# Kernel tuning notes

Measured on AMD Instinct MI355X. Metric: run time of the kernel, lower is better.

Reference implementation:

```python
import jax, jax.numpy as jnp
import numpy as np

N_NODES = 40000
N_EDGES = 400000
N_GRAPHS = 64
CONV_DIM = 64
N_FEAT = 9
EDGE_DIM = 3
Z_DIM = 2 * CONV_DIM + EDGE_DIM  # 131


def setup_inputs() -> dict:
    key = jax.random.key(0)
    ks = jax.random.split(key, 32)
    def lin(k, fan_in, fan_out):
        b = 1.0 / np.sqrt(fan_in)
        kw, kb = jax.random.split(k)
        return (jax.random.uniform(kw, (fan_in, fan_out), jnp.float32, -b, b),
                jax.random.uniform(kb, (fan_out,), jnp.float32, -b, b))
    inp = {}
    inp['x'] = jax.random.normal(ks[0], (N_NODES, N_FEAT), jnp.float32)
    inp['edge_index_1'] = jax.random.randint(ks[1], (2, N_EDGES), 0, N_NODES, jnp.int32)
    inp['edge_index_2'] = jax.random.randint(ks[2], (2, N_EDGES), 0, N_NODES, jnp.int32)
    inp['weight_1'] = jax.random.normal(ks[3], (N_EDGES, EDGE_DIM), jnp.float32)
    inp['weight_2'] = jax.random.normal(ks[4], (N_EDGES, EDGE_DIM), jnp.float32)
    # sorted graph ids: 64 graphs of 625 nodes each
    inp['batch'] = jnp.repeat(jnp.arange(N_GRAPHS, dtype=jnp.int32), N_NODES // N_GRAPHS)
    # parameters (stored [in, out])
    inp['fc1_w'], inp['fc1_b'] = lin(ks[5], N_FEAT, CONV_DIM)
    inp['lin_f_w'], inp['lin_f_b'] = lin(ks[6], Z_DIM, CONV_DIM)
    inp['lin_s_w'], inp['lin_s_b'] = lin(ks[7], Z_DIM, CONV_DIM)
    inp['gru_w_ih'], inp['gru_b_ih'] = lin(ks[8], CONV_DIM, 3 * CONV_DIM)  # gate order r,z,n
    inp['gru_w_hh'], inp['gru_b_hh'] = lin(ks[9], CONV_DIM, 3 * CONV_DIM)
    inp['fcs_w'], inp['fcs_b'] = lin(ks[10], CONV_DIM, CONV_DIM)
    inp['fc2c_w'], inp['fc2c_b'] = lin(ks[11], CONV_DIM, 64)
    inp['fc3c_w'], inp['fc3c_b'] = lin(ks[12], 64, 2)
    inp['fc2d_w'], inp['fc2d_b'] = lin(ks[13], CONV_DIM, 64)
    inp['fc3d_w'], inp['fc3d_b'] = lin(ks[14], 64, 2)
    return inp


def _cgconv(x, edge_index, edge_attr, wf, bf, ws, bs):
    # CGConv, flow='target_to_source': x_i = x[row], x_j = x[col], aggregate (mean) at row
    row, col = edge_index[0], edge_index[1]
    z = jnp.concatenate([x[row], x[col], edge_attr], axis=-1)       # [E, 131]
    msg = jax.nn.sigmoid(z @ wf + bf) * jax.nn.softplus(z @ ws + bs)  # [E, C]
    agg = jax.ops.segment_sum(msg, row, num_segments=x.shape[0])
    cnt = jax.ops.segment_sum(jnp.ones((msg.shape[0],), msg.dtype), row, num_segments=x.shape[0])
    return x + agg / jnp.maximum(cnt, 1.0)[:, None]                  # residual


def _gru_step(xt, h, w_ih, w_hh, b_ih, b_hh):
    gi = xt @ w_ih + b_ih
    gh = h @ w_hh + b_hh
    ir, iz, inn = jnp.split(gi, 3, axis=-1)
    hr, hz, hn = jnp.split(gh, 3, axis=-1)
    r = jax.nn.sigmoid(ir + hr)
    zg = jax.nn.sigmoid(iz + hz)
    n = jnp.tanh(inn + r * hn)
    return (1.0 - zg) * n + zg * h


def reference(x, edge_index_1, edge_index_2, weight_1, weight_2, batch,
              fc1_w, fc1_b, lin_f_w, lin_f_b, lin_s_w, lin_s_b,
              gru_w_ih, gru_b_ih, gru_w_hh, gru_b_hh,
              fcs_w, fcs_b, fc2c_w, fc2c_b, fc3c_w, fc3c_b,
              fc2d_w, fc2d_b, fc3d_w, fc3d_b):
    x = jax.nn.relu(x @ fc1_w + fc1_b)          # dropout inactive (eval)
    h = x
    for _ in range(3):                          # 3 GRU refinement iterations
        m = jax.nn.relu(_cgconv(x, edge_index_2, weight_2, lin_f_w, lin_f_b, lin_s_w, lin_s_b))
        m = jax.nn.relu(_cgconv(m, edge_index_1, weight_1, lin_f_w, lin_f_b, lin_s_w, lin_s_b))
        h = _gru_step(m, h, gru_w_ih, gru_w_hh, gru_b_ih, gru_b_hh)
        x = h
    # first node index of each graph (batch is sorted)
    idx_ct = jnp.searchsorted(batch, jnp.arange(N_GRAPHS, dtype=batch.dtype))
    xg = x[idx_ct]                              # [B, C]
    xg = jax.nn.relu(xg @ fcs_w + fcs_b)
    xc = jax.nn.relu(xg @ fc2c_w + fc2c_b)
    x_class = jax.nn.sigmoid(xc @ fc3c_w + fc3c_b)
    xd = jax.nn.relu(xg @ fc2d_w + fc2d_b)
    x_delta = xd @ fc3d_w + fc3d_b
    return (x_class, x_delta)
```

## Files before the change

kernel.cpp:

```cpp
#include <hip/hip_runtime.h>
#include <hip/hip_bf16.h>
#include <hip/hip_fp16.h>
#include <math.h>

constexpr int NE = 400000;
constexpr int NN = 40000;
constexpr int CD = 64;
constexpr int NGRAPH = 64;
constexpr int SCAN_BLOCKS = (NN + 255) / 256;
constexpr int EBLK = (NE + 255) / 256;

typedef _Float16 f16x8 __attribute__((ext_vector_type(8)));
typedef float f32x4 __attribute__((ext_vector_type(4)));

__global__ void k_fc1(const float* __restrict__ x,
                      const float* __restrict__ w,
                      const float* __restrict__ b,
                      float* __restrict__ out) {
    int i = blockIdx.x * 256 + threadIdx.x;
    if (i >= NN * CD) return;
    int n = i >> 6, c = i & 63;
    float acc = b[c];
    #pragma unroll
    for (int k = 0; k < 9; ++k)
        acc = fmaf(x[n * 9 + k], w[k * 64 + c], acc);
    out[i] = fmaxf(acc, 0.f);
}

__global__ void k_count2(const int* __restrict__ ei1, const int* __restrict__ ei2,
                         int* __restrict__ cnt1, int* __restrict__ cnt2) {
    const int b = blockIdx.x;
    const bool s2 = (b >= EBLK);
    const int* ei = s2 ? ei2 : ei1;
    int* cnt = s2 ? cnt2 : cnt1;
    int e = (s2 ? b - EBLK : b) * 256 + threadIdx.x;
    if (e >= NE) return;
    atomicAdd(&cnt[ei[e]], 1);
}

__global__ void k_scan_part2(const int* __restrict__ cnt1, const int* __restrict__ cnt2,
                             int* __restrict__ part1, int* __restrict__ part2) {
    __shared__ int red[256];
    const int b = blockIdx.x;
    const bool s2 = (b >= SCAN_BLOCKS);
    const int* cnt = s2 ? cnt2 : cnt1;
    int* partials = s2 ? part2 : part1;
    const int bb = s2 ? b - SCAN_BLOCKS : b;
    const int tid = threadIdx.x;
    const int i = bb * 256 + tid;
    red[tid] = (i < NN) ? cnt[i] : 0;
    __syncthreads();
    for (int s = 128; s > 0; s >>= 1) {
        if (tid < s) red[tid] += red[tid + s];
        __syncthreads();
    }
    if (tid == 0) partials[bb] = red[0];
}

__global__ void k_scan_mid2(const int* __restrict__ part1, const int* __restrict__ part2,
                            int* __restrict__ offs1, int* __restrict__ offs2) {
    __shared__ int part[256];
    const bool s2 = (blockIdx.x == 1);
    const int* partials = s2 ? part2 : part1;
    int* offs = s2 ? offs2 : offs1;
    const int tid = threadIdx.x;
    const int v = (tid < SCAN_BLOCKS) ? partials[tid] : 0;
    part[tid] = v;
    __syncthreads();
    for (int off = 1; off < 256; off <<= 1) {
        int t = (tid >= off) ? part[tid - off] : 0;
        __syncthreads();
        part[tid] += t;
        __syncthreads();
    }
    if (tid < SCAN_BLOCKS) offs[tid] = part[tid] - v;
}

__global__ void k_scan_fill2(const int* __restrict__ cnt1, const int* __restrict__ cnt2,
                             const int* __restrict__ offs1, const int* __restrict__ offs2,
                             int* __restrict__ rs1, int* __restrict__ rs2,
                             int* __restrict__ cur1, int* __restrict__ cur2) {
    __shared__ int part[256];
    const int b = blockIdx.x;
    const bool s2 = (b >= SCAN_BLOCKS);
    const int* cnt = s2 ? cnt2 : cnt1;
    const int* offs = s2 ? offs2 : offs1;
    int* row_start = s2 ? rs2 : rs1;
    int* cursor = s2 ? cur2 : cur1;
    const int bb = s2 ? b - SCAN_BLOCKS : b;
    const int tid = threadIdx.x;
    const int i = bb * 256 + tid;
    const int v = (i < NN) ? cnt[i] : 0;
    part[tid] = v;
    __syncthreads();
    for (int off = 1; off < 256; off <<= 1) {
        int t = (tid >= off) ? part[tid - off] : 0;
        __syncthreads();
        part[tid] += t;
        __syncthreads();
    }
    const int excl = part[tid] - v + offs[bb];
    if (i < NN) { row_start[i] = excl; cursor[i] = excl; }
    if (i == NN - 1) row_start[NN] = NE;
}

__global__ void k_scatgath2(const int* __restrict__ ei1, const int* __restrict__ ei2,
                            const float* __restrict__ w1, const float* __restrict__ w2,
                            int* __restrict__ cur1, int* __restrict__ cur2,
                            int2* __restrict__ rcP1, int2* __restrict__ rcP2,
                            float4* __restrict__ ewP1, float4* __restrict__ ewP2) {
    const int b = blockIdx.x;
    const bool s2 = (b >= EBLK);
    const int* ei = s2 ? ei2 : ei1;
    const float* ew = s2 ? w2 : w1;
    int* cursor = s2 ? cur2 : cur1;
    int2* rcP = s2 ? rcP2 : rcP1;
    float4* ewP = s2 ? ewP2 : ewP1;
    int e = (s2 ? b - EBLK : b) * 256 + threadIdx.x;
    if (e >= NE) return;
    const int r = ei[e];
    const int c = ei[NE + e];
    const int pos = atomicAdd(&cursor[r], 1);
    rcP[pos] = make_int2(r, c);
    ewP[pos] = make_float4(ew[3 * e], ew[3 * e + 1], ew[3 * e + 2], 0.f);
}

__global__ void k_wt16(const float* __restrict__ lfw, const float* __restrict__ lsw,
                       _Float16* __restrict__ Wt) {
    const int k = blockIdx.x;
    const int c = threadIdx.x;
    float v;
    if (c < 64)       v = lfw[k * 64 + c];
    else if (c < 128) v = lsw[k * 64 + (c - 64)];
    else if (c < 192) v = lfw[(64 + k) * 64 + (c - 128)];
    else              v = lsw[(64 + k) * 64 + (c - 192)];
    Wt[c * 64 + k] = (_Float16)v;
}

__global__ void k_wtg16(const float* __restrict__ wih, const float* __restrict__ whh,
                        _Float16* __restrict__ WtG) {
    const int i = blockIdx.x * 256 + threadIdx.x;
    const int c = i >> 6, k = i & 63;
    const float v = (c < 192) ? wih[k * 192 + c] : whh[k * 192 + (c - 192)];
    WtG[c * 64 + k] = (_Float16)v;
}

__launch_bounds__(256, 4)
__global__ void k_proj_mfma(const float* __restrict__ x,
                            const _Float16* __restrict__ Wt,
                            const float* __restrict__ bfp, const float* __restrict__ bsp,
                            float* __restrict__ Pi, __half2* __restrict__ Pj16) {
    __shared__ _Float16 xs16[32][72];
    const int tid = threadIdx.x;
    const int n0 = blockIdx.x * 32;
    {
        const int n = tid >> 3, k0 = (tid & 7) * 8;
        const float4 a = *(const float4*)&x[(size_t)(n0 + n) * 64 + k0];
        const float4 b = *(const float4*)&x[(size_t)(n0 + n) * 64 + k0 + 4];
        f16x8 v;
        v[0] = (_Float16)a.x; v[1] = (_Float16)a.y; v[2] = (_Float16)a.z; v[3] = (_Float16)a.w;
        v[4] = (_Float16)b.x; v[5] = (_Float16)b.y; v[6] = (_Float16)b.z; v[7] = (_Float16)b.w;
        *(f16x8*)&xs16[n][k0] = v;
    }
    __syncthreads();
    const int l  = tid & 63;
    const int w  = tid >> 6;
    const int lr = l & 15;
    const int kb = l >> 4;
    const int nt = w & 1;
    const f16x8 A0 = *(const f16x8*)&xs16[nt * 16 + lr][kb * 8];
    const f16x8 A1 = *(const f16x8*)&xs16[nt * 16 + lr][32 + kb * 8];
    const int orow = n0 + nt * 16 + kb * 4;

    if (w < 2) {
        for (int ct = 0; ct < 8; ++ct) {
            const int col = ct * 16 + lr;
            const f16x8 B0 = *(const f16x8*)&Wt[col * 64 + kb * 8];
            const f16x8 B1 = *(const f16x8*)&Wt[col * 64 + 32 + kb * 8];
            f32x4 acc = {0.f, 0.f, 0.f, 0.f};
            acc = __builtin_amdgcn_mfma_f32_16x16x32_f16(A0, B0, acc, 0, 0, 0);
            acc = __builtin_amdgcn_mfma_f32_16x16x32_f16(A1, B1, acc, 0, 0, 0);
            const float bias = (col < 64) ? bfp[col] : bsp[col - 64];
            #pragma unroll
            for (int r = 0; r < 4; ++r)
                Pi[(size_t)(orow + r) * 128 + col] = acc[r] + bias;
        }
    } else {
        for (int pt = 0; pt < 4; ++pt) {
            const int colF = 128 + pt * 16 + lr;
            const int colS = 192 + pt * 16 + lr;
            const f16x8 BF0 = *(const f16x8*)&Wt[colF * 64 + kb * 8];
            const f16x8 BF1 = *(const f16x8*)&Wt[colF * 64 + 32 + kb * 8];
            const f16x8 BS0 = *(const f16x8*)&Wt[colS * 64 + kb * 8];
            const f16x8 BS1 = *(const f16x8*)&Wt[colS * 64 + 32 + kb * 8];
            f32x4 aF = {0.f, 0.f, 0.f, 0.f}, aS = {0.f, 0.f, 0.f, 0.f};
            aF = __builtin_amdgcn_mfma_f32_16x16x32_f16(A0, BF0, aF, 0, 0, 0);
            aF = __builtin_amdgcn_mfma_f32_16x16x32_f16(A1, BF1, aF, 0, 0, 0);
            aS = __builtin_amdgcn_mfma_f32_16x16x32_f16(A0, BS0, aS, 0, 0, 0);
            aS = __builtin_amdgcn_mfma_f32_16x16x32_f16(A1, BS1, aS, 0, 0, 0);
            const int cj = pt * 16 + lr;
            #pragma unroll
            for (int r = 0; r < 4; ++r)
                Pj16[(size_t)(orow + r) * 64 + cj] = __floats2half2_rn((float)aF[r], (float)aS[r]);
        }
    }
}

__launch_bounds__(256, 8)
__global__ void k_edge_range(const __half2* __restrict__ Pj,
                             const float* __restrict__ Pi,
                             const int2* __restrict__ rcP, const float4* __restrict__ ewP,
                             const float* __restrict__ wfe, const float* __restrict__ wse,
                             const int* __restrict__ rs,
                             const float* __restrict__ xin, float* __restrict__ out) {
    __shared__ __align__(8) __half2 piH[8][64];
    __shared__ __align__(16) float accS[8][8][64];
    __shared__ int rsS[9];
    const int tid = threadIdx.x;
    const int hw = tid >> 5;
    const int hb = hw & 1;
    const int wv = tid >> 6;
    const int c2 = (tid & 31) * 2;
    const int r0 = blockIdx.x * 8;
    for (int i = tid; i < 512; i += 256) {
        const int row = i >> 6, ch = i & 63;
        piH[row][ch] = __floats2half2_rn(Pi[(size_t)(r0 + row) * 128 + ch],
                                         Pi[(size_t)(r0 + row) * 128 + 64 + ch]);
    }
    for (int i = tid; i < 4096; i += 256)
        ((float*)accS)[i] = 0.f;
    if (tid < 9) rsS[tid] = rs[r0 + tid];
    __syncthreads();
    const float wf0a = wfe[c2],       wf0b = wfe[c2 + 1];
    const float wf1a = wfe[64 + c2],  wf1b = wfe[64 + c2 + 1];
    const float wf2a = wfe[128 + c2], wf2b = wfe[128 + c2 + 1];
    const float ws0a = wse[c2],       ws0b = wse[c2 + 1];
    const float ws1a = wse[64 + c2],  ws1b = wse[64 + c2 + 1];
    const float ws2a = wse[128 + c2], ws2b = wse[128 + c2 + 1];
    const int pbeg = rsS[0], pend = rsS[8];

#define EDGE_BODY(P)                                                              \
    {                                                                             \
        const int2 rc = rcP[P];                                                   \
        const float4 e = ewP[P];                                                  \
        const uint2 Jraw = *(const uint2*)&Pj[rc.y * 64 + c2];                    \
        const float2 Ja = __half22float2(*(const __half2*)&Jraw.x);               \
        const float2 Jb = __half22float2(*(const __half2*)&Jraw.y);               \
        const int row = rc.x - r0;                                                \
        const uint2 PH = *(const uint2*)&piH[row][c2];                            \
        const float2 Pa = __half22float2(*(const __half2*)&PH.x);                 \
        const float2 Pb = __half22float2(*(const __half2*)&PH.y);                 \
        const float afa = Pa.x + Ja.x + e.x * wf0a + e.y * wf1a + e.z * wf2a;     \
        const float asa = Pa.y + Ja.y + e.x * ws0a + e.y * ws1a + e.z * ws2a;     \
        const float afb = Pb.x + Jb.x + e.x * wf0b + e.y * wf1b + e.z * wf2b;     \
        const float asb = Pb.y + Jb.y + e.x * ws0b + e.y * ws1b + e.z * ws2b;     \
        const float sga = 1.f / (1.f + __expf(-afa));                             \
        const float spa = (asa > 20.f) ? asa : __logf(1.f + __expf(asa));         \
        const float sgb = 1.f / (1.f + __expf(-afb));                             \
        const float spb = (asb > 20.f) ? asb : __logf(1.f + __expf(asb));         \
        float2 acc = *(const float2*)&accS[hw][row][c2];                          \
        acc.x = fmaf(sga, spa, acc.x);                                            \
        acc.y = fmaf(sgb, spb, acc.y);                                            \
        *(float2*)&accS[hw][row][c2] = acc;                                       \
    }

    int p0 = pbeg + 2 * wv;
    #pragma unroll 2
    for (; p0 + 2 <= pend; p0 += 8) {
        const int p = p0 + hb;
        EDGE_BODY(p)
    }
    {
        const int p = p0 + hb;
        if (p < pend) EDGE_BODY(p)
    }
#undef EDGE_BODY

    __syncthreads();
    for (int i = tid; i < 512; i += 256) {
        const int row = i >> 6, ch = i & 63;
        float s = 0.f;
        #pragma unroll
        for (int a = 0; a < 8; ++a) s += accS[a][row][ch];
        const int deg = rsS[row + 1] - rsS[row];
        const size_t o = (size_t)(r0 + row) * 64 + ch;
        out[o] = fmaxf(fmaf(s, 1.f / (float)max(deg, 1), xin[o]), 0.f);
    }
}

__global__ void k_gru_mfma(const float* __restrict__ m, float* __restrict__ h,
                           const _Float16* __restrict__ WtG,
                           const float* __restrict__ bih, const float* __restrict__ bhh) {
    __shared__ _Float16 ms16[32][72];
    __shared__ _Float16 hs16[32][72];
    __shared__ __align__(16) float hs32[32][64];
    const int tid = threadIdx.x;
    const int n0 = blockIdx.x * 32;
    {
        const int n = tid >> 3, k0 = (tid & 7) * 8;
        const float4 ma = *(const float4*)&m[(size_t)(n0 + n) * 64 + k0];
        const float4 mb = *(const float4*)&m[(size_t)(n0 + n) * 64 + k0 + 4];
        const float4 ha = *(const float4*)&h[(size_t)(n0 + n) * 64 + k0];
        const float4 hb = *(const float4*)&h[(size_t)(n0 + n) * 64 + k0 + 4];
        f16x8 mv, hv;
        mv[0] = (_Float16)ma.x; mv[1] = (_Float16)ma.y; mv[2] = (_Float16)ma.z; mv[3] = (_Float16)ma.w;
        mv[4] = (_Float16)mb.x; mv[5] = (_Float16)mb.y; mv[6] = (_Float16)mb.z; mv[7] = (_Float16)mb.w;
        hv[0] = (_Float16)ha.x; hv[1] = (_Float16)ha.y; hv[2] = (_Float16)ha.z; hv[3] = (_Float16)ha.w;
        hv[4] = (_Float16)hb.x; hv[5] = (_Float16)hb.y; hv[6] = (_Float16)hb.z; hv[7] = (_Float16)hb.w;
        *(f16x8*)&ms16[n][k0] = mv;
        *(f16x8*)&hs16[n][k0] = hv;
        *(float4*)&hs32[n][k0] = ha;
        *(float4*)&hs32[n][k0 + 4] = hb;
    }
    __syncthreads();
    const int l  = tid & 63;
    const int w  = tid >> 6;
    const int lr = l & 15;
    const int kb = l >> 4;
    const int nt = w & 1;
    const int cg = w >> 1;
    const f16x8 A0 = *(const f16x8*)&ms16[nt * 16 + lr][kb * 8];
    const f16x8 A1 = *(const f16x8*)&ms16[nt * 16 + lr][32 + kb * 8];
    const f16x8 H0 = *(const f16x8*)&hs16[nt * 16 + lr][kb * 8];
    const f16x8 H1 = *(const f16x8*)&hs16[nt * 16 + lr][32 + kb * 8];
    const int orow = n0 + nt * 16 + kb * 4;
    const int lrow = nt * 16 + kb * 4;

    #pragma unroll
    for (int t = 0; t < 2; ++t) {
        const int ct = cg + t * 2;
        const int c = ct * 16 + lr;
        const f16x8 BiR0 = *(const f16x8*)&WtG[(c)       * 64 + kb * 8];
        const f16x8 BiR1 = *(const f16x8*)&WtG[(c)       * 64 + 32 + kb * 8];
        const f16x8 BiZ0 = *(const f16x8*)&WtG[(64 + c)  * 64 + kb * 8];
        const f16x8 BiZ1 = *(const f16x8*)&WtG[(64 + c)  * 64 + 32 + kb * 8];
        const f16x8 BiN0 = *(const f16x8*)&WtG[(128 + c) * 64 + kb * 8];
        const f16x8 BiN1 = *(const f16x8*)&WtG[(128 + c) * 64 + 32 + kb * 8];
        const f16x8 BhR0 = *(const f16x8*)&WtG[(192 + c) * 64 + kb * 8];
        const f16x8 BhR1 = *(const f16x8*)&WtG[(192 + c) * 64 + 32 + kb * 8];
        const f16x8 BhZ0 = *(const f16x8*)&WtG[(256 + c) * 64 + kb * 8];
        const f16x8 BhZ1 = *(const f16x8*)&WtG[(256 + c) * 64 + 32 + kb * 8];
        const f16x8 BhN0 = *(const f16x8*)&WtG[(320 + c) * 64 + kb * 8];
        const f16x8 BhN1 = *(const f16x8*)&WtG[(320 + c) * 64 + 32 + kb * 8];
        f32x4 aIR = {0,0,0,0}, aIZ = {0,0,0,0}, aIN = {0,0,0,0};
        f32x4 aHR = {0,0,0,0}, aHZ = {0,0,0,0}, aHN = {0,0,0,0};
        aIR = __builtin_amdgcn_mfma_f32_16x16x32_f16(A0, BiR0, aIR, 0, 0, 0);
        aIR = __builtin_amdgcn_mfma_f32_16x16x32_f16(A1, BiR1, aIR, 0, 0, 0);
        aIZ = __builtin_amdgcn_mfma_f32_16x16x32_f16(A0, BiZ0, aIZ, 0, 0, 0);
        aIZ = __builtin_amdgcn_mfma_f32_16x16x32_f16(A1, BiZ1, aIZ, 0, 0, 0);
        aIN = __builtin_amdgcn_mfma_f32_16x16x32_f16(A0, BiN0, aIN, 0, 0, 0);
        aIN = __builtin_amdgcn_mfma_f32_16x16x32_f16(A1, BiN1, aIN, 0, 0, 0);
        aHR = __builtin_amdgcn_mfma_f32_16x16x32_f16(H0, BhR0, aHR, 0, 0, 0);
        aHR = __builtin_amdgcn_mfma_f32_16x16x32_f16(H1, BhR1, aHR, 0, 0, 0);
        aHZ = __builtin_amdgcn_mfma_f32_16x16x32_f16(H0, BhZ0, aHZ, 0, 0, 0);
        aHZ = __builtin_amdgcn_mfma_f32_16x16x32_f16(H1, BhZ1, aHZ, 0, 0, 0);
        aHN = __builtin_amdgcn_mfma_f32_16x16x32_f16(H0, BhN0, aHN, 0, 0, 0);
        aHN = __builtin_amdgcn_mfma_f32_16x16x32_f16(H1, BhN1, aHN, 0, 0, 0);
        const float bir = bih[c], biz = bih[64 + c], bin = bih[128 + c];
        const float bhr = bhh[c], bhz = bhh[64 + c], bhn = bhh[128 + c];
        #pragma unroll
        for (int r = 0; r < 4; ++r) {
            const float rg = 1.f / (1.f + __expf(-(((float)aIR[r] + bir) + ((float)aHR[r] + bhr))));
            const float zg = 1.f / (1.f + __expf(-(((float)aIZ[r] + biz) + ((float)aHZ[r] + bhz))));
            const float ng = tanhf(((float)aIN[r] + bin) + rg * ((float)aHN[r] + bhn));
            h[(size_t)(orow + r) * 64 + c] = (1.f - zg) * ng + zg * hs32[lrow + r][c];
        }
    }
}

__global__ void k_head(const float* __restrict__ h, const int* __restrict__ batch,
                       const float* __restrict__ fcsw, const float* __restrict__ fcsb,
                       const float* __restrict__ f2cw, const float* __restrict__ f2cb,
                       const float* __restrict__ f3cw, const float* __restrict__ f3cb,
                       const float* __restrict__ f2dw, const float* __restrict__ f2db,
                       const float* __restrict__ f3dw, const float* __restrict__ f3db,
                       float* __restrict__ out) {
    __shared__ float hsB[4096];
    __shared__ float waB[4096];
    __shared__ float wbB[4096];
    __shared__ float wcB[4096];
    __shared__ int sidx[64];
    const int tid = threadIdx.x;
    if (tid < 64) {
        int lo = 0, hi = NN;
        while (lo < hi) {
            int mid = (lo + hi) >> 1;
            if (batch[mid] < tid) lo = mid + 1; else hi = mid;
        }
        sidx[tid] = lo;
    }
    __syncthreads();
    for (int i = tid; i < 4096; i += 256) {
        int g = i >> 6, k = i & 63;
        hsB[i] = h[(size_t)sidx[g] * 64 + k];
        waB[i] = fcsw[i];
        wbB[i] = f2cw[i];
        wcB[i] = f2dw[i];
    }
    __syncthreads();
    float v[16];
    #pragma unroll
    for (int j = 0; j < 16; ++j) {
        const int i = j * 256 + tid, g = i >> 6, c = i & 63;
        float a = fcsb[c];
        for (int k = 0; k < 64; ++k) a = fmaf(hsB[g * 64 + k], waB[k * 64 + c], a);
        v[j] = fmaxf(a, 0.f);
    }
    __syncthreads();
    #pragma unroll
    for (int j = 0; j < 16; ++j) hsB[j * 256 + tid] = v[j];
    __syncthreads();
    float vc[16], vd[16];
    #pragma unroll
    for (int j = 0; j < 16; ++j) {
        const int i = j * 256 + tid, g = i >> 6, c = i & 63;
        float a1 = f2cb[c], a2 = f2db[c];
        for (int k = 0; k < 64; ++k) {
            const float xv = hsB[g * 64 + k];
            a1 = fmaf(xv, wbB[k * 64 + c], a1);
            a2 = fmaf(xv, wcB[k * 64 + c], a2);
        }
        vc[j] = fmaxf(a1, 0.f);
        vd[j] = fmaxf(a2, 0.f);
    }
    __syncthreads();
    #pragma unroll
    for (int j = 0; j < 16; ++j) {
        waB[j * 256 + tid] = vc[j];
        wbB[j * 256 + tid] = vd[j];
    }
    if (tid < 128) wcB[tid] = f3cw[tid];
    else           wcB[tid] = f3dw[tid - 128];
    __syncthreads();
    if (tid < 128) {
        int g = tid >> 1, j = tid & 1;
        float a = f3cb[j];
        for (int k = 0; k < 64; ++k) a = fmaf(waB[g * 64 + k], wcB[k * 2 + j], a);
        out[g * 2 + j] = 1.f / (1.f + expf(-a));
    } else {
        int t = tid - 128, g = t >> 1, j = t & 1;
        float a = f3db[j];
        for (int k = 0; k < 64; ++k) a = fmaf(wbB[g * 64 + k], wcB[128 + k * 2 + j], a);
        out[128 + g * 2 + j] = a;
    }
}

extern "C" void kernel_launch(void* const* d_in, const int* in_sizes, int n_in,
                              void* d_out, int out_size, void* d_ws, size_t ws_size,
                              hipStream_t stream) {
    (void)in_sizes; (void)n_in; (void)out_size; (void)ws_size;
    const float* x    = (const float*)d_in[0];
    const int* ei1    = (const int*)d_in[1];
    const int* ei2    = (const int*)d_in[2];
    const float* w1   = (const float*)d_in[3];
    const float* w2   = (const float*)d_in[4];
    const int* batch  = (const int*)d_in[5];
    const float* fc1w = (const float*)d_in[6];
    const float* fc1b = (const float*)d_in[7];
    const float* lfw  = (const float*)d_in[8];
    const float* lfb  = (const float*)d_in[9];
    const float* lsw  = (const float*)d_in[10];
    const float* lsb  = (const float*)d_in[11];
    const float* wih  = (const float*)d_in[12];
    const float* bih  = (const float*)d_in[13];
    const float* whh  = (const float*)d_in[14];
    const float* bhh  = (const float*)d_in[15];
    const float* fcsw = (const float*)d_in[16];
    const float* fcsb = (const float*)d_in[17];
    const float* f2cw = (const float*)d_in[18];
    const float* f2cb = (const float*)d_in[19];
    const float* f3cw = (const float*)d_in[20];
    const float* f3cb = (const float*)d_in[21];
    const float* f2dw = (const float*)d_in[22];
    const float* f2db = (const float*)d_in[23];
    const float* f3dw = (const float*)d_in[24];
    const float* f3db = (const float*)d_in[25];

    char* ws = (char*)d_ws;
    size_t off = 0;
    auto alloc = [&](size_t bytes) { char* p = ws + off; off += (bytes + 255) & ~size_t(255); return p; };
    float*   Pi    = (float*)alloc(size_t(NN) * 128 * 4);
    __half2* Pj16  = (__half2*)alloc(size_t(NN) * 64 * 4);
    float*   hbuf  = (float*)alloc(size_t(NN) * CD * 4);
    float*   mbuf  = (float*)alloc(size_t(NN) * CD * 4);
    _Float16* W16  = (_Float16*)alloc(256 * 64 * 2);
    _Float16* WG16 = (_Float16*)alloc(384 * 64 * 2);
    int*   cnt1  = (int*)alloc(size_t(NN) * 4);
    int*   cnt2  = (int*)alloc(size_t(NN) * 4);
    int*   rs1   = (int*)alloc(size_t(NN + 1) * 4);
    int*   rs2   = (int*)alloc(size_t(NN + 1) * 4);
    int*   cur1  = (int*)alloc(size_t(NN + 1) * 4);
    int*   cur2  = (int*)alloc(size_t(NN + 1) * 4);
    int2*  rcP1  = (int2*)alloc(size_t(NE) * 8);
    int2*  rcP2  = (int2*)alloc(size_t(NE) * 8);
    float4* ewP1 = (float4*)alloc(size_t(NE) * 16);
    float4* ewP2 = (float4*)alloc(size_t(NE) * 16);
    int*   part1 = (int*)alloc(256 * 4);
    int*   part2 = (int*)alloc(256 * 4);
    int*   offs1 = (int*)alloc(256 * 4);
    int*   offs2 = (int*)alloc(256 * 4);

    const int NB_NC = (NN * CD + 255) / 256;
    const int EDGE_BLOCKS = NN / 8;
    const int PROJ_BLOCKS = NN / 32;
    const int GRU_BLOCKS  = NN / 32;

    const float* lfe = lfw + 128 * 64;
    const float* lse = lsw + 128 * 64;

    hipMemsetAsync(cnt1, 0, size_t(NN) * 4 * 2 + 256, stream);
    k_count2<<<2 * EBLK, 256, 0, stream>>>(ei1, ei2, cnt1, cnt2);
    k_scan_part2<<<2 * SCAN_BLOCKS, 256, 0, stream>>>(cnt1, cnt2, part1, part2);
    k_scan_mid2<<<2, 256, 0, stream>>>(part1, part2, offs1, offs2);
    k_scan_fill2<<<2 * SCAN_BLOCKS, 256, 0, stream>>>(cnt1, cnt2, offs1, offs2, rs1, rs2, cur1, cur2);
    k_scatgath2<<<2 * EBLK, 256, 0, stream>>>(ei1, ei2, w1, w2, cur1, cur2,
                                              rcP1, rcP2, ewP1, ewP2);
    k_wt16<<<64, 256, 0, stream>>>(lfw, lsw, W16);
    k_wtg16<<<96, 256, 0, stream>>>(wih, whh, WG16);

    k_fc1<<<NB_NC, 256, 0, stream>>>(x, fc1w, fc1b, hbuf);

    for (int it = 0; it < 3; ++it) {
        k_proj_mfma<<<PROJ_BLOCKS, 256, 0, stream>>>(hbuf, W16, lfb, lsb, Pi, Pj16);
        k_edge_range<<<EDGE_BLOCKS, 256, 0, stream>>>(Pj16, Pi, rcP2, ewP2,
                                                      lfe, lse, rs2, hbuf, mbuf);
        k_proj_mfma<<<PROJ_BLOCKS, 256, 0, stream>>>(mbuf, W16, lfb, lsb, Pi, Pj16);
        k_edge_range<<<EDGE_BLOCKS, 256, 0, stream>>>(Pj16, Pi, rcP1, ewP1,
                                                      lfe, lse, rs1, mbuf, mbuf);
        k_gru_mfma<<<GRU_BLOCKS, 256, 0, stream>>>(mbuf, hbuf, WG16, bih, bhh);
    }

    k_head<<<1, 256, 0, stream>>>(hbuf, batch, fcsw, fcsb, f2cw, f2cb, f3cw, f3cb,
                                  f2dw, f2db, f3dw, f3db, (float*)d_out);
}
```

Before: 563.2 us.

## Pack sorted edge records into compact int and fp16 edge-weight arrays

The CSR preprocessing is split into a scatter pass that writes only an edge permutation and a gather pass that writes packed records sequentially. Each record stores the column index with the row's offset within its 8-row block in the top bits, plus the edge weights as fp16 in 8 bytes instead of a float4. The aim is to cut the per-edge bytes read by the six edge kernels from 24 to 12 and to make the scattered writes smaller. In exchange there is one extra preprocessing kernel, the edge weights lose precision, and the column index must fit in 28 bits.

```diff
diff --git a/kernel.cpp b/kernel.cpp
--- a/kernel.cpp
+++ b/kernel.cpp
@@ -104,25 +104,44 @@
     if (i == NN - 1) row_start[NN] = NE;
 }
 
-__global__ void k_scatgath2(const int* __restrict__ ei1, const int* __restrict__ ei2,
-                            const float* __restrict__ w1, const float* __restrict__ w2,
-                            int* __restrict__ cur1, int* __restrict__ cur2,
-                            int2* __restrict__ rcP1, int2* __restrict__ rcP2,
-                            float4* __restrict__ ewP1, float4* __restrict__ ewP2) {
+__global__ void k_scatter2(const int* __restrict__ ei1, const int* __restrict__ ei2,
+                           int* __restrict__ cur1, int* __restrict__ cur2,
+                           int* __restrict__ perm1, int* __restrict__ perm2) {
+    const int b = blockIdx.x;
+    const bool s2 = (b >= EBLK);
+    const int* ei = s2 ? ei2 : ei1;
+    int* cursor = s2 ? cur2 : cur1;
+    int* perm = s2 ? perm2 : perm1;
+    int e = (s2 ? b - EBLK : b) * 256 + threadIdx.x;
+    if (e >= NE) return;
+    int pos = atomicAdd(&cursor[ei[e]], 1);
+    perm[pos] = e;
+}
+
+__global__ void k_gather2(const int* __restrict__ ei1, const int* __restrict__ ei2,
+                          const float* __restrict__ w1, const float* __restrict__ w2,
+                          const int* __restrict__ perm1, const int* __restrict__ perm2,
+                          int* __restrict__ pk1, int* __restrict__ pk2,
+                          uint2* __restrict__ ewH1, uint2* __restrict__ ewH2) {
     const int b = blockIdx.x;
     const bool s2 = (b >= EBLK);
     const int* ei = s2 ? ei2 : ei1;
     const float* ew = s2 ? w2 : w1;
-    int* cursor = s2 ? cur2 : cur1;
-    int2* rcP = s2 ? rcP2 : rcP1;
-    float4* ewP = s2 ? ewP2 : ewP1;
-    int e = (s2 ? b - EBLK : b) * 256 + threadIdx.x;
-    if (e >= NE) return;
+    const int* perm = s2 ? perm2 : perm1;
+    int* pk = s2 ? pk2 : pk1;
+    uint2* ewH = s2 ? ewH2 : ewH1;
+    int p = (s2 ? b - EBLK : b) * 256 + threadIdx.x;
+    if (p >= NE) return;
+    const int e = perm[p];
     const int r = ei[e];
     const int c = ei[NE + e];
-    const int pos = atomicAdd(&cursor[r], 1);
-    rcP[pos] = make_int2(r, c);
-    ewP[pos] = make_float4(ew[3 * e], ew[3 * e + 1], ew[3 * e + 2], 0.f);
+    pk[p] = ((r & 7) << 28) | c;
+    const __half2 h01 = __floats2half2_rn(ew[3 * e], ew[3 * e + 1]);
+    const __half2 h2  = __floats2half2_rn(ew[3 * e + 2], 0.f);
+    uint2 u;
+    u.x = *(const unsigned*)&h01;
+    u.y = *(const unsigned*)&h2;
+    ewH[p] = u;
 }
 
 __global__ void k_wt16(const float* __restrict__ lfw, const float* __restrict__ lsw,
@@ -209,7 +228,7 @@
 __launch_bounds__(256, 8)
 __global__ void k_edge_range(const __half2* __restrict__ Pj,
                              const float* __restrict__ Pi,
-                             const int2* __restrict__ rcP, const float4* __restrict__ ewP,
+                             const int* __restrict__ pk, const uint2* __restrict__ ewH,
                              const float* __restrict__ wfe, const float* __restrict__ wse,
                              const int* __restrict__ rs,
                              const float* __restrict__ xin, float* __restrict__ out) {
@@ -241,19 +260,22 @@
 
 #define EDGE_BODY(P)                                                              \
     {                                                                             \
-        const int2 rc = rcP[P];                                                   \
-        const float4 e = ewP[P];                                                  \
-        const uint2 Jraw = *(const uint2*)&Pj[rc.y * 64 + c2];                    \
+        const unsigned pkv = (unsigned)pk[P];                                     \
+        const uint2 eh = ewH[P];                                                  \
+        const float2 e01 = __half22float2(*(const __half2*)&eh.x);                \
+        const float2 e2x = __half22float2(*(const __half2*)&eh.y);                \
+        const int row = pkv >> 28;                                                \
+        const int col = pkv & 0x0FFFFFFF;                                         \
+        const uint2 Jraw = *(const uint2*)&Pj[(size_t)col * 64 + c2];             \
         const float2 Ja = __half22float2(*(const __half2*)&Jraw.x);               \
         const float2 Jb = __half22float2(*(const __half2*)&Jraw.y);               \
-        const int row = rc.x - r0;                                                \
         const uint2 PH = *(const uint2*)&piH[row][c2];                            \
         const float2 Pa = __half22float2(*(const __half2*)&PH.x);                 \
         const float2 Pb = __half22float2(*(const __half2*)&PH.y);                 \
-        const float afa = Pa.x + Ja.x + e.x * wf0a + e.y * wf1a + e.z * wf2a;     \
-        const float asa = Pa.y + Ja.y + e.x * ws0a + e.y * ws1a + e.z * ws2a;     \
-        const float afb = Pb.x + Jb.x + e.x * wf0b + e.y * wf1b + e.z * wf2b;     \
-        const float asb = Pb.y + Jb.y + e.x * ws0b + e.y * ws1b + e.z * ws2b;     \
+        const float afa = Pa.x + Ja.x + e01.x * wf0a + e01.y * wf1a + e2x.x * wf2a; \
+        const float asa = Pa.y + Ja.y + e01.x * ws0a + e01.y * ws1a + e2x.x * ws2a; \
+        const float afb = Pb.x + Jb.x + e01.x * wf0b + e01.y * wf1b + e2x.x * wf2b; \
+        const float asb = Pb.y + Jb.y + e01.x * ws0b + e01.y * ws1b + e2x.x * ws2b; \
         const float sga = 1.f / (1.f + __expf(-afa));                             \
         const float spa = (asa > 20.f) ? asa : __logf(1.f + __expf(asa));         \
         const float sgb = 1.f / (1.f + __expf(-afb));                             \
@@ -491,10 +513,12 @@
     int*   rs2   = (int*)alloc(size_t(NN + 1) * 4);
     int*   cur1  = (int*)alloc(size_t(NN + 1) * 4);
     int*   cur2  = (int*)alloc(size_t(NN + 1) * 4);
-    int2*  rcP1  = (int2*)alloc(size_t(NE) * 8);
-    int2*  rcP2  = (int2*)alloc(size_t(NE) * 8);
-    float4* ewP1 = (float4*)alloc(size_t(NE) * 16);
-    float4* ewP2 = (float4*)alloc(size_t(NE) * 16);
+    int*   perm1 = (int*)alloc(size_t(NE) * 4);
+    int*   perm2 = (int*)alloc(size_t(NE) * 4);
+    int*   pk1   = (int*)alloc(size_t(NE) * 4);
+    int*   pk2   = (int*)alloc(size_t(NE) * 4);
+    uint2* ewH1  = (uint2*)alloc(size_t(NE) * 8);
+    uint2* ewH2  = (uint2*)alloc(size_t(NE) * 8);
     int*   part1 = (int*)alloc(256 * 4);
     int*   part2 = (int*)alloc(256 * 4);
     int*   offs1 = (int*)alloc(256 * 4);
@@ -513,8 +537,9 @@
     k_scan_part2<<<2 * SCAN_BLOCKS, 256, 0, stream>>>(cnt1, cnt2, part1, part2);
     k_scan_mid2<<<2, 256, 0, stream>>>(part1, part2, offs1, offs2);
     k_scan_fill2<<<2 * SCAN_BLOCKS, 256, 0, stream>>>(cnt1, cnt2, offs1, offs2, rs1, rs2, cur1, cur2);
-    k_scatgath2<<<2 * EBLK, 256, 0, stream>>>(ei1, ei2, w1, w2, cur1, cur2,
-                                              rcP1, rcP2, ewP1, ewP2);
+    k_scatter2<<<2 * EBLK, 256, 0, stream>>>(ei1, ei2, cur1, cur2, perm1, perm2);
+    k_gather2<<<2 * EBLK, 256, 0, stream>>>(ei1, ei2, w1, w2, perm1, perm2,
+                                            pk1, pk2, ewH1, ewH2);
     k_wt16<<<64, 256, 0, stream>>>(lfw, lsw, W16);
     k_wtg16<<<96, 256, 0, stream>>>(wih, whh, WG16);
 
@@ -522,10 +547,10 @@
 
     for (int it = 0; it < 3; ++it) {
         k_proj_mfma<<<PROJ_BLOCKS, 256, 0, stream>>>(hbuf, W16, lfb, lsb, Pi, Pj16);
-        k_edge_range<<<EDGE_BLOCKS, 256, 0, stream>>>(Pj16, Pi, rcP2, ewP2,
+        k_edge_range<<<EDGE_BLOCKS, 256, 0, stream>>>(Pj16, Pi, pk2, ewH2,
                                                       lfe, lse, rs2, hbuf, mbuf);
         k_proj_mfma<<<PROJ_BLOCKS, 256, 0, stream>>>(mbuf, W16, lfb, lsb, Pi, Pj16);
-        k_edge_range<<<EDGE_BLOCKS, 256, 0, stream>>>(Pj16, Pi, rcP1, ewP1,
+        k_edge_range<<<EDGE_BLOCKS, 256, 0, stream>>>(Pj16, Pi, pk1, ewH1,
                                                       lfe, lse, rs1, mbuf, mbuf);
         k_gru_mfma<<<GRU_BLOCKS, 256, 0, stream>>>(mbuf, hbuf, WG16, bih, bhh);
     }
```

After: 581.3 us. 1.03x slower.
